# Performance work log

Hardware: AMD Instinct MI355X
Metric: run time of the kernel (lower is better)

The kernel has to match this reference:

```python
import jax, jax.numpy as jnp
import numpy as np

RADIUS = 0.1
NUM_POINT = 1024  # M centroids
SAMPLE_NUM = 32   # K neighbors per ball


def fps(xyz, m):
    """D-FPS farthest point sampling. xyz: (B,N,3) -> idx (B,m) int32."""
    B, N, _ = xyz.shape

    def step(carry, _):
        mind, far = carry  # mind (B,N), far (B,)
        centroid = jnp.take_along_axis(xyz, far[:, None, None], axis=1)  # (B,1,3)
        d = jnp.sum((xyz - centroid) ** 2, axis=-1)  # (B,N)
        mind = jnp.minimum(mind, d)
        nxt = jnp.argmax(mind, axis=1).astype(jnp.int32)
        return (mind, nxt), far

    init = (jnp.full((B, N), jnp.inf, xyz.dtype), jnp.zeros((B,), jnp.int32))
    _, idx = jax.lax.scan(step, init, None, length=m)
    return jnp.transpose(idx)  # (B,m)


def ball_query(new_xyz, xyz, radius, k):
    """First-k points within radius of each centroid, padded with first hit.
    new_xyz (B,M,3), xyz (B,N,3) -> (B,M,k) int32."""
    N = xyz.shape[1]
    d2 = jnp.sum((new_xyz[:, :, None, :] - xyz[:, None, :, :]) ** 2, axis=-1)  # (B,M,N)
    order = jnp.where(d2 < radius * radius, jnp.arange(N, dtype=jnp.int32)[None, None, :], N)
    neg, pos = jax.lax.top_k(-order, k)  # k smallest 'order' values -> first-k in-ball indices
    valid = (-neg) < N
    return jnp.where(valid, pos, pos[..., :1])


def setup_inputs() -> dict:
    key = jax.random.key(0)
    ks = jax.random.split(key, 12)
    B, N, C = 4, 16384, 64
    Cin = C + 3  # use_xyz=True
    points_xyz = jax.random.uniform(ks[0], (B, N, 3), dtype=jnp.float32)
    features = jax.random.normal(ks[1], (B, C, N), dtype=jnp.float32)
    s = lambda fan: 1.0 / np.sqrt(fan)
    inp = {
        "points_xyz": points_xyz,
        "features": features,
        "Wa": jax.random.normal(ks[2], (128, Cin), jnp.float32) * s(Cin),
        "ba": jnp.zeros((128,), jnp.float32),
        "Wb": jax.random.normal(ks[3], (128, 128), jnp.float32) * s(128),
        "bb": jnp.zeros((128,), jnp.float32),
        "Ws": jax.random.normal(ks[4], (128, Cin), jnp.float32) * s(Cin),
        "bs": jnp.zeros((128,), jnp.float32),
        "Wc": jax.random.normal(ks[5], (512, 128), jnp.float32) * s(128),
        "bc": jnp.zeros((512,), jnp.float32),
        "Wd": jax.random.normal(ks[6], (128, 512), jnp.float32) * s(512),
        "bd": jnp.zeros((128,), jnp.float32),
    }
    return inp


def _conv1x1(W, b, x):
    # pointwise conv over (B,C,M,K)
    return jnp.einsum('oc,bcmk->bomk', W, x) + b[None, :, None, None]


def reference(points_xyz, features, Wa, ba, Wb, bb, Ws, bs, Wc, bc, Wd, bd):
    idx = fps(points_xyz, NUM_POINT)  # (B,M)
    new_xyz = jnp.take_along_axis(points_xyz, idx[:, :, None], axis=1)  # (B,M,3)
    nidx = ball_query(new_xyz, points_xyz, RADIUS, SAMPLE_NUM)  # (B,M,K)
    # gather and relativize grouped xyz; gather grouped features
    grouped_xyz = jax.vmap(lambda p, i: p[i])(points_xyz, nidx) - new_xyz[:, :, None, :]  # (B,M,K,3)
    gfeat = jax.vmap(lambda f, i: f[:, i])(features, nidx)  # (B,C,M,K)
    g = jnp.concatenate([jnp.transpose(grouped_xyz, (0, 3, 1, 2)), gfeat], axis=1)  # (B,3+C,M,K)
    # mlp + shortcut residual + relu
    h = _conv1x1(Wb, bb, jax.nn.relu(_conv1x1(Wa, ba, g)))
    h = jax.nn.relu(h + _conv1x1(Ws, bs, g))
    # inverted mlp + identity residual + relu
    inv = _conv1x1(Wd, bd, jax.nn.relu(_conv1x1(Wc, bc, h)))
    out = jax.nn.relu(inv + h)
    pooled = jnp.max(out, axis=-1)  # max pool over K -> (B,128,M)
    return new_xyz, pooled, idx
```

## Files before the change

### kernel.cpp

```cpp
#include <hip/hip_runtime.h>

#define N_PTS   16384
#define M_CENT  1024
#define K_SMP   32
#define C_FEAT  64
#define NCELL   512

using bf16x8 = __attribute__((ext_vector_type(8))) short;
using s16x4  = __attribute__((ext_vector_type(4))) short;
using f32x4  = __attribute__((ext_vector_type(4))) float;

__device__ inline short f2bf(float f) {
    unsigned u = __float_as_uint(f);
    u += 0x7fffu + ((u >> 16) & 1u);
    return (short)(u >> 16);
}

#define DPP_SHR1 0x111
#define DPP_SHR2 0x112
#define DPP_SHR4 0x114
#define DPP_SHR8 0x118
#define DPP_BC15 0x142
#define DPP_BC31 0x143

template<int CTRL, int RM>
__device__ __forceinline__ float dppmax(float v) {
    int o = __builtin_amdgcn_update_dpp(__float_as_int(v), __float_as_int(v),
                                        CTRL, RM, 0xF, false);
    return fmaxf(v, __int_as_float(o));
}

__device__ __forceinline__ float wave64_fmax(float v) {
    v = dppmax<DPP_SHR1, 0xF>(v);
    v = dppmax<DPP_SHR2, 0xF>(v);
    v = dppmax<DPP_SHR4, 0xF>(v);
    v = dppmax<DPP_SHR8, 0xF>(v);
    v = dppmax<DPP_BC15, 0xA>(v);
    v = dppmax<DPP_BC31, 0xC>(v);
    return __int_as_float(__builtin_amdgcn_readlane(__float_as_int(v), 63));
}

__device__ __forceinline__ float row16_fmax(float v) {
    v = dppmax<DPP_SHR1, 0xF>(v);
    v = dppmax<DPP_SHR2, 0xF>(v);
    v = dppmax<DPP_SHR4, 0xF>(v);
    v = dppmax<DPP_SHR8, 0xF>(v);
    return __int_as_float(__builtin_amdgcn_readlane(__float_as_int(v), 15));
}

__device__ inline int hcell_of(float x, float y, float z) {
    int xi = (int)(x * 8.0f); xi = xi < 0 ? 0 : (xi > 7 ? 7 : xi);
    int yi = (int)(y * 8.0f); yi = yi < 0 ? 0 : (yi > 7 ? 7 : yi);
    int zi = (int)(z * 8.0f); zi = zi < 0 ? 0 : (zi > 7 ? 7 : zi);
    unsigned X[3] = {(unsigned)xi, (unsigned)yi, (unsigned)zi};
#pragma unroll
    for (unsigned Q = 4; Q > 1; Q >>= 1) {
        unsigned P = Q - 1;
#pragma unroll
        for (int i = 0; i < 3; ++i) {
            if (X[i] & Q) X[0] ^= P;
            else { unsigned t = (X[0] ^ X[i]) & P; X[0] ^= t; X[i] ^= t; }
        }
    }
    X[1] ^= X[0]; X[2] ^= X[1];
    unsigned t = 0;
#pragma unroll
    for (unsigned Q = 4; Q > 1; Q >>= 1)
        if (X[2] & Q) t ^= Q - 1;
    X[0] ^= t; X[1] ^= t; X[2] ^= t;
    int h = 0;
#pragma unroll
    for (int q = 2; q >= 0; --q)
        h = (h << 3) | (((X[0] >> q) & 1) << 2) | (((X[1] >> q) & 1) << 1) | ((X[2] >> q) & 1);
    return h;
}

__global__ __launch_bounds__(1024) void hist_kernel(
    const float* __restrict__ xyz, int* __restrict__ ghist)
{
    __shared__ int h[NCELL];
    const int b = blockIdx.x, tid = threadIdx.x;
    if (tid < NCELL) h[tid] = 0;
    __syncthreads();
    const float* P = xyz + (size_t)b * N_PTS * 3;
    for (int i = 0; i < 16; ++i) {
        const int p = tid + (i << 10);
        atomicAdd(&h[hcell_of(P[p*3], P[p*3+1], P[p*3+2])], 1);
    }
    __syncthreads();
    if (tid < NCELL) ghist[b * NCELL + tid] = h[tid];
}

__global__ __launch_bounds__(NCELL) void scan_kernel(
    const int* __restrict__ ghist, int* __restrict__ gbase)
{
    __shared__ int h[NCELL];
    const int b = blockIdx.x, t = threadIdx.x;
    h[t] = ghist[b * NCELL + t];
    __syncthreads();
    int s = 0;
    for (int i = 0; i < t; ++i) s += h[i];
    gbase[b * NCELL + t] = s;
}

__global__ __launch_bounds__(1024) void scatter_kernel(
    const float* __restrict__ xyz, int* __restrict__ gbase,
    float4* __restrict__ gsxyz)
{
    const int b = blockIdx.x, tid = threadIdx.x;
    const float* P = xyz + (size_t)b * N_PTS * 3;
    for (int i = 0; i < 16; ++i) {
        const int p = tid + (i << 10);
        float x = P[p*3], y = P[p*3+1], z = P[p*3+2];
        int c = hcell_of(x, y, z);
        int pos = atomicAdd(&gbase[b * NCELL + c], 1);
        gsxyz[(size_t)b * N_PTS + pos] = make_float4(x, y, z, __int_as_float(p));
    }
}

__global__ __launch_bounds__(1024) void fps_kernel(
    const float* __restrict__ xyz,
    const float4* __restrict__ gsxyz,
    float* __restrict__ newxyz_out,
    float* __restrict__ idxf_out)
{
#pragma clang fp contract(off)
    const int b = blockIdx.x, tid = threadIdx.x;
    const int wid = tid >> 6, lane = tid & 63;
    const float4* S = gsxyz + (size_t)b * N_PTS;

    __shared__ float2 xy[16 * 1024];
    __shared__ unsigned long long wkeys[2][16];
    __shared__ float4 wcoord[2][16];

    float z[16], mind[16];
    unsigned npk[8];
    float lox = 1e30f, hix = -1e30f, loy = 1e30f, hiy = -1e30f, loz = 1e30f, hiz = -1e30f;
#pragma unroll
    for (int i = 0; i < 16; ++i) {
        const float4 v = S[tid * 16 + i];
        xy[i * 1024 + tid] = make_float2(v.x, v.y);
        z[i] = v.z;
        mind[i] = __int_as_float(0x7f800000);
        const unsigned nr = 16383u - (unsigned)__float_as_int(v.w);
        if (i & 1) npk[i >> 1] |= nr << 16;
        else       npk[i >> 1]  = nr;
        lox = fminf(lox, v.x); hix = fmaxf(hix, v.x);
        loy = fminf(loy, v.y); hiy = fmaxf(hiy, v.y);
        loz = fminf(loz, v.z); hiz = fmaxf(hiz, v.z);
    }
    const unsigned pbx = (__float_as_uint(lox) >> 16) |
                         ((((__float_as_uint(hix) + 0xFFFFu) >> 16) << 16));
    const unsigned pby = (__float_as_uint(loy) >> 16) |
                         ((((__float_as_uint(hiy) + 0xFFFFu) >> 16) << 16));
    const unsigned pbz = (__float_as_uint(loz) >> 16) |
                         ((((__float_as_uint(hiz) + 0xFFFFu) >> 16) << 16));

    const float* P = xyz + (size_t)b * N_PTS * 3;
    float cx = P[0], cy = P[1], cz = P[2];
    if (tid == 0) {
        idxf_out[b * M_CENT] = 0.0f;
        newxyz_out[(b * M_CENT) * 3 + 0] = cx;
        newxyz_out[(b * M_CENT) * 3 + 1] = cy;
        newxyz_out[(b * M_CENT) * 3 + 2] = cz;
    }
    __syncthreads();

    float lmax = __int_as_float(0x7f800000);
    unsigned cwk_hi = 0u, cwk_lo = 0u;
    float cwx = 0.f, cwy = 0.f, cwz = 0.f;

    for (int j = 1; j < M_CENT; ++j) {
        const int par = j & 1;
        const float blox = __uint_as_float(pbx << 16);
        const float bhix = __uint_as_float(pbx & 0xFFFF0000u);
        const float bloy = __uint_as_float(pby << 16);
        const float bhiy = __uint_as_float(pby & 0xFFFF0000u);
        const float bloz = __uint_as_float(pbz << 16);
        const float bhiz = __uint_as_float(pbz & 0xFFFF0000u);
        float tx = fmaxf(fmaxf(blox - cx, cx - bhix), 0.0f);
        float ty = fmaxf(fmaxf(bloy - cy, cy - bhiy), 0.0f);
        float tz = fmaxf(fmaxf(bloz - cz, cz - bhiz), 0.0f);
        float lb = (tx * tx + ty * ty) + tz * tz;
        bool need = (lb * 0.999985f) < lmax;

        if (__any(need)) {
            float bv0 = -1.0f, bv1 = -1.0f;
#pragma unroll
            for (int i = 0; i < 16; i += 2) {
                const float2 p0 = xy[i * 1024 + tid];
                const float2 p1 = xy[(i + 1) * 1024 + tid];
                float dx0 = p0.x - cx, dy0 = p0.y - cy, dz0 = z[i] - cz;
                float dx1 = p1.x - cx, dy1 = p1.y - cy, dz1 = z[i + 1] - cz;
                float d0 = (dx0 * dx0 + dy0 * dy0) + dz0 * dz0;
                float d1 = (dx1 * dx1 + dy1 * dy1) + dz1 * dz1;
                float m0 = fminf(mind[i], d0);
                float m1 = fminf(mind[i + 1], d1);
                mind[i] = m0; mind[i + 1] = m1;
                bv0 = fmaxf(bv0, m0);
                bv1 = fmaxf(bv1, m1);
            }
            const float bv = fmaxf(bv0, bv1);
            lmax = bv;
            unsigned bk = 0u; float wz = 0.f;
#pragma unroll
            for (int i = 0; i < 16; ++i) {
                const unsigned nr = (i & 1) ? (npk[i >> 1] >> 16)
                                            : (npk[i >> 1] & 0xFFFFu);
                const unsigned nk = (nr << 4) | (unsigned)i;
                const bool c = (mind[i] == bv) && (nk >= bk);
                bk = c ? nk : bk;
                wz = c ? z[i] : wz;
            }
            const float wmax = wave64_fmax(bv);
            unsigned long long m = __ballot(bv == wmax);
            unsigned bestnk = 0u; int ol = 0;
            while (m) {
                const int l = (int)__ffsll(m) - 1;
                m &= m - 1;
                const unsigned nkl = (unsigned)__builtin_amdgcn_readlane((int)bk, l);
                if (nkl >= bestnk) { bestnk = nkl; ol = l; }
            }
            cwk_hi = __float_as_uint(wmax);
            cwk_lo = ((bestnk >> 4) << 8) | ((unsigned)wid << 4);
            const float2 pw = xy[(bestnk & 15u) * 1024 + (wid << 6) + ol];
            cwx = pw.x; cwy = pw.y;
            cwz = __int_as_float(__builtin_amdgcn_readlane(__float_as_int(wz), ol));
        }
        if (lane == 0) {
            wkeys[par][wid]  = ((unsigned long long)cwk_hi << 32) | cwk_lo;
            wcoord[par][wid] = make_float4(cwx, cwy, cwz, 0.f);
        }
        __syncthreads();

        const unsigned long long k = wkeys[par][lane & 15];
        const float vkey = __uint_as_float((unsigned)(k >> 32));
        const float vmax = row16_fmax(vkey);
        unsigned long long mm = __ballot(vkey == vmax) & 0xFFFFull;
        unsigned bestlo = 0u;
        while (mm) {
            const int l = (int)__ffsll(mm) - 1;
            mm &= mm - 1;
            const unsigned lo = (unsigned)__builtin_amdgcn_readlane((int)(unsigned)k, l);
            if (lo >= bestlo) bestlo = lo;
        }
        const int winw = (int)((bestlo >> 4) & 15u);
        const float4 wc = wcoord[par][winw];
        cx = wc.x; cy = wc.y; cz = wc.z;
        if (tid == 0) {
            const int orig = 16383 - (int)(bestlo >> 8);
            idxf_out[b * M_CENT + j] = (float)orig;
            newxyz_out[(b * M_CENT + j) * 3 + 0] = cx;
            newxyz_out[(b * M_CENT + j) * 3 + 1] = cy;
            newxyz_out[(b * M_CENT + j) * 3 + 2] = cz;
        }
    }
}

__global__ __launch_bounds__(256) void ball_kernel(
    const float* __restrict__ xyz,
    const float* __restrict__ newxyz,
    int* __restrict__ nidx)
{
#pragma clang fp contract(off)
    const float R2 = (float)(0.1 * 0.1);
    const int gw   = blockIdx.x * 4 + (threadIdx.x >> 6);
    const int lane = threadIdx.x & 63;
    const int b    = gw >> 10;
    const float* P = xyz + (size_t)b * N_PTS * 3;
    const float cx = newxyz[gw * 3 + 0];
    const float cy = newxyz[gw * 3 + 1];
    const float cz = newxyz[gw * 3 + 2];
    int* out = nidx + gw * K_SMP;

    int cnt = 0, first = -1;
    for (int base = 0; base < N_PTS; base += 64) {
        const int n = base + lane;
        float dx = P[n * 3 + 0] - cx;
        float dy = P[n * 3 + 1] - cy;
        float dz = P[n * 3 + 2] - cz;
        float xx = dx * dx, yy = dy * dy, zz = dz * dz;
        float d2 = (xx + yy) + zz;
        bool inb = d2 < R2;
        unsigned long long mask = __ballot(inb);
        if (mask) {
            if (first < 0) first = base + __ffsll(mask) - 1;
            int before = __popcll(mask & ((1ull << lane) - 1ull));
            int slot = cnt + before;
            if (inb && slot < K_SMP) out[slot] = n;
            cnt += __popcll(mask);
            if (cnt >= K_SMP) break;
        }
    }
    for (int s = cnt + lane; s < K_SMP; s += 64) out[s] = first;
}

__global__ void prep_w(const float* __restrict__ src, short* __restrict__ dst,
                       int OC, int IC, int ICP, int remap)
{
    int i = blockIdx.x * 256 + threadIdx.x;
    if (i >= OC * ICP) return;
    int oc = i / ICP, ic = i - oc * ICP;
    float v = 0.0f;
    if (remap) {
        if (ic < 64)      v = src[oc * IC + 3 + ic];
        else if (ic < 67) v = src[oc * IC + (ic - 64)];
    } else if (ic < IC)   v = src[oc * IC + ic];
    dst[i] = f2bf(v);
}

__global__ __launch_bounds__(256) void tfeat_kernel(
    const float* __restrict__ feat, float* __restrict__ featT)
{
    __shared__ float t[64][65];
    const int b = blockIdx.y;
    const int n0 = blockIdx.x * 64;
    for (int it = 0; it < 16; ++it) {
        int idx = it * 256 + threadIdx.x;
        int c = idx >> 6, n = idx & 63;
        t[c][n] = feat[((size_t)b * 64 + c) * N_PTS + n0 + n];
    }
    __syncthreads();
    for (int it = 0; it < 16; ++it) {
        int idx = it * 256 + threadIdx.x;
        int n = idx >> 6, c = idx & 63;
        featT[((size_t)b * N_PTS + n0 + n) * 64 + c] = t[c][n];
    }
}

__global__ __launch_bounds__(256, 2) void mlp_kernel(
    const float* __restrict__ xyz, const float* __restrict__ feat,
    const float* __restrict__ featT, int useT,
    const float* __restrict__ newxyz, const int* __restrict__ nidx,
    const short* __restrict__ WaB, const float* __restrict__ ba,
    const short* __restrict__ WbB, const float* __restrict__ bb,
    const short* __restrict__ WsB, const float* __restrict__ bs,
    const short* __restrict__ WcB, const float* __restrict__ bc,
    const short* __restrict__ WdB, const float* __restrict__ bd,
    float* __restrict__ pooled)
{
    __shared__ short Xt[64][104];
    __shared__ short Ht[64][136];
    __shared__ short Tt[64][136];

    const int tid = threadIdx.x;
    const int w = tid >> 6, l = tid & 63, l16 = l & 15, kg = l >> 4;
    const int cen0 = blockIdx.x * 2;
    const int b = cen0 >> 10;
    const int ocw = 32 * w;

    {
        const int col = tid >> 2, part = tid & 3;
        const int ci = cen0 + (col >> 5);
        const int nn = nidx[ci * K_SMP + (col & 31)];
        float v[16];
        if (useT) {
            const f32x4* src = (const f32x4*)(featT + ((size_t)b * N_PTS + nn) * 64 + part * 16);
            f32x4 f0 = src[0], f1 = src[1], f2 = src[2], f3 = src[3];
            v[0]=f0[0]; v[1]=f0[1]; v[2]=f0[2]; v[3]=f0[3];
            v[4]=f1[0]; v[5]=f1[1]; v[6]=f1[2]; v[7]=f1[3];
            v[8]=f2[0]; v[9]=f2[1]; v[10]=f2[2]; v[11]=f2[3];
            v[12]=f3[0]; v[13]=f3[1]; v[14]=f3[2]; v[15]=f3[3];
        } else {
            const float* F = feat + (size_t)b * C_FEAT * N_PTS + nn;
#pragma unroll
            for (int q = 0; q < 16; ++q) v[q] = F[(size_t)(part * 16 + q) * N_PTS];
        }
        bf16x8 h0, h1;
#pragma unroll
        for (int q = 0; q < 8; ++q) { h0[q] = f2bf(v[q]); h1[q] = f2bf(v[q + 8]); }
        *(bf16x8*)&Xt[col][part * 16]     = h0;
        *(bf16x8*)&Xt[col][part * 16 + 8] = h1;
        if (part == 0) {
            bf16x8 hx, zv;
#pragma unroll
            for (int q = 0; q < 8; ++q) { hx[q] = 0; zv[q] = 0; }
            hx[0] = f2bf(xyz[((size_t)b * N_PTS + nn) * 3 + 0] - newxyz[ci * 3 + 0]);
            hx[1] = f2bf(xyz[((size_t)b * N_PTS + nn) * 3 + 1] - newxyz[ci * 3 + 1]);
            hx[2] = f2bf(xyz[((size_t)b * N_PTS + nn) * 3 + 2] - newxyz[ci * 3 + 2]);
            *(bf16x8*)&Xt[col][64] = hx;
            *(bf16x8*)&Xt[col][72] = zv;
            *(bf16x8*)&Xt[col][80] = zv;
            *(bf16x8*)&Xt[col][88] = zv;
        }
    }
    __syncthreads();

    f32x4 accA[2][4], accS[2][4];
#pragma unroll
    for (int o = 0; o < 2; ++o)
#pragma unroll
        for (int ct = 0; ct < 4; ++ct) {
#pragma unroll
            for (int r = 0; r < 4; ++r) { accA[o][ct][r] = 0.f; accS[o][ct][r] = 0.f; }
        }
#pragma unroll
    for (int k = 0; k < 3; ++k) {
        bf16x8 xb[4];
#pragma unroll
        for (int ct = 0; ct < 4; ++ct)
            xb[ct] = *(const bf16x8*)&Xt[ct * 16 + l16][k * 32 + kg * 8];
#pragma unroll
        for (int o = 0; o < 2; ++o) {
            const int row = ocw + o * 16 + l16;
            bf16x8 wa  = *(const bf16x8*)(WaB + row * 96 + k * 32 + kg * 8);
            bf16x8 wsv = *(const bf16x8*)(WsB + row * 96 + k * 32 + kg * 8);
#pragma unroll
            for (int ct = 0; ct < 4; ++ct) {
                accA[o][ct] = __builtin_amdgcn_mfma_f32_16x16x32_bf16(wa,  xb[ct], accA[o][ct], 0, 0, 0);
                accS[o][ct] = __builtin_amdgcn_mfma_f32_16x16x32_bf16(wsv, xb[ct], accS[o][ct], 0, 0, 0);
            }
        }
    }
#pragma unroll
    for (int o = 0; o < 2; ++o) {
        const f32x4 bav = *(const f32x4*)(ba + ocw + o * 16 + kg * 4);
#pragma unroll
        for (int ct = 0; ct < 4; ++ct) {
            s16x4 hv;
#pragma unroll
            for (int r = 0; r < 4; ++r) hv[r] = f2bf(fmaxf(accA[o][ct][r] + bav[r], 0.f));
            *(s16x4*)&Ht[ct * 16 + l16][ocw + o * 16 + kg * 4] = hv;
        }
    }
    __syncthreads();

    f32x4 accB[2][4];
#pragma unroll
    for (int o = 0; o < 2; ++o)
#pragma unroll
        for (int ct = 0; ct < 4; ++ct) {
#pragma unroll
            for (int r = 0; r < 4; ++r) accB[o][ct][r] = 0.f;
        }
#pragma unroll
    for (int k = 0; k < 4; ++k) {
        bf16x8 xb[4];
#pragma unroll
        for (int ct = 0; ct < 4; ++ct)
            xb[ct] = *(const bf16x8*)&Ht[ct * 16 + l16][k * 32 + kg * 8];
#pragma unroll
        for (int o = 0; o < 2; ++o) {
            const int row = ocw + o * 16 + l16;
            bf16x8 wbv = *(const bf16x8*)(WbB + row * 128 + k * 32 + kg * 8);
#pragma unroll
            for (int ct = 0; ct < 4; ++ct)
                accB[o][ct] = __builtin_amdgcn_mfma_f32_16x16x32_bf16(wbv, xb[ct], accB[o][ct], 0, 0, 0);
        }
    }
    f32x4 hreg[2][4];
#pragma unroll
    for (int o = 0; o < 2; ++o) {
        const f32x4 bbv = *(const f32x4*)(bb + ocw + o * 16 + kg * 4);
        const f32x4 bsv = *(const f32x4*)(bs + ocw + o * 16 + kg * 4);
#pragma unroll
        for (int ct = 0; ct < 4; ++ct) {
#pragma unroll
            for (int r = 0; r < 4; ++r)
                hreg[o][ct][r] = fmaxf((accB[o][ct][r] + bbv[r]) + (accS[o][ct][r] + bsv[r]), 0.f);
        }
    }
    __syncthreads();
#pragma unroll
    for (int o = 0; o < 2; ++o)
#pragma unroll
        for (int ct = 0; ct < 4; ++ct) {
            s16x4 hv;
#pragma unroll
            for (int r = 0; r < 4; ++r) hv[r] = f2bf(hreg[o][ct][r]);
            *(s16x4*)&Ht[ct * 16 + l16][ocw + o * 16 + kg * 4] = hv;
        }
    __syncthreads();

    f32x4 accD[2][4];
#pragma unroll
    for (int o = 0; o < 2; ++o)
#pragma unroll
        for (int ct = 0; ct < 4; ++ct) {
#pragma unroll
            for (int r = 0; r < 4; ++r) accD[o][ct][r] = 0.f;
        }
    for (int cc = 0; cc < 4; ++cc) {
        f32x4 accC[2][4];
#pragma unroll
        for (int o = 0; o < 2; ++o)
#pragma unroll
            for (int ct = 0; ct < 4; ++ct) {
#pragma unroll
                for (int r = 0; r < 4; ++r) accC[o][ct][r] = 0.f;
            }
#pragma unroll
        for (int k = 0; k < 4; ++k) {
            bf16x8 xb[4];
#pragma unroll
            for (int ct = 0; ct < 4; ++ct)
                xb[ct] = *(const bf16x8*)&Ht[ct * 16 + l16][k * 32 + kg * 8];
#pragma unroll
            for (int o = 0; o < 2; ++o) {
                const int row = cc * 128 + ocw + o * 16 + l16;
                bf16x8 wcv = *(const bf16x8*)(WcB + row * 128 + k * 32 + kg * 8);
#pragma unroll
                for (int ct = 0; ct < 4; ++ct)
                    accC[o][ct] = __builtin_amdgcn_mfma_f32_16x16x32_bf16(wcv, xb[ct], accC[o][ct], 0, 0, 0);
            }
        }
        __syncthreads();
#pragma unroll
        for (int o = 0; o < 2; ++o) {
            const f32x4 bcv = *(const f32x4*)(bc + cc * 128 + ocw + o * 16 + kg * 4);
#pragma unroll
            for (int ct = 0; ct < 4; ++ct) {
                s16x4 tv;
#pragma unroll
                for (int r = 0; r < 4; ++r) tv[r] = f2bf(fmaxf(accC[o][ct][r] + bcv[r], 0.f));
                *(s16x4*)&Tt[ct * 16 + l16][ocw + o * 16 + kg * 4] = tv;
            }
        }
        __syncthreads();
#pragma unroll
        for (int k = 0; k < 4; ++k) {
            bf16x8 tb[4];
#pragma unroll
            for (int ct = 0; ct < 4; ++ct)
                tb[ct] = *(const bf16x8*)&Tt[ct * 16 + l16][k * 32 + kg * 8];
#pragma unroll
            for (int o = 0; o < 2; ++o) {
                const int row = ocw + o * 16 + l16;
                bf16x8 wdv = *(const bf16x8*)(WdB + row * 512 + cc * 128 + k * 32 + kg * 8);
#pragma unroll
                for (int ct = 0; ct < 4; ++ct)
                    accD[o][ct] = __builtin_amdgcn_mfma_f32_16x16x32_bf16(wdv, tb[ct], accD[o][ct], 0, 0, 0);
            }
        }
    }

    const int m0 = cen0 & 1023;
#pragma unroll
    for (int o = 0; o < 2; ++o) {
        const f32x4 bdv = *(const f32x4*)(bd + ocw + o * 16 + kg * 4);
#pragma unroll
        for (int r = 0; r < 4; ++r) {
            float a0 = fmaxf((accD[o][0][r] + bdv[r]) + hreg[o][0][r], 0.f);
            float a1 = fmaxf((accD[o][1][r] + bdv[r]) + hreg[o][1][r], 0.f);
            float a2 = fmaxf((accD[o][2][r] + bdv[r]) + hreg[o][2][r], 0.f);
            float a3 = fmaxf((accD[o][3][r] + bdv[r]) + hreg[o][3][r], 0.f);
            float u0 = fmaxf(a0, a1), u1 = fmaxf(a2, a3);
#pragma unroll
            for (int off = 1; off < 16; off <<= 1) {
                u0 = fmaxf(u0, __shfl_xor(u0, off));
                u1 = fmaxf(u1, __shfl_xor(u1, off));
            }
            if (l16 == 0) {
                const int oc = ocw + o * 16 + kg * 4 + r;
                pooled[((size_t)b * 128 + oc) * 1024 + m0]     = u0;
                pooled[((size_t)b * 128 + oc) * 1024 + m0 + 1] = u1;
            }
        }
    }
}

extern "C" void kernel_launch(void* const* d_in, const int* in_sizes, int n_in,
                              void* d_out, int out_size, void* d_ws, size_t ws_size,
                              hipStream_t stream)
{
    const float* xyz  = (const float*)d_in[0];
    const float* feat = (const float*)d_in[1];
    const float* Wa = (const float*)d_in[2];   const float* ba = (const float*)d_in[3];
    const float* Wb = (const float*)d_in[4];   const float* bb = (const float*)d_in[5];
    const float* Ws = (const float*)d_in[6];   const float* bs = (const float*)d_in[7];
    const float* Wc = (const float*)d_in[8];   const float* bc = (const float*)d_in[9];
    const float* Wd = (const float*)d_in[10];  const float* bd = (const float*)d_in[11];

    float* out    = (float*)d_out;
    float* newxyz = out;
    float* pooled = out + 4 * 1024 * 3;
    float* idxf   = pooled + 4 * 128 * 1024;

    char* ws = (char*)d_ws;
    float4* gsxyz = (float4*)ws;
    int*    nidx  = (int*)ws;
    short* WaB = (short*)(ws + (1 << 20));
    short* WsB = WaB + 128 * 96;
    short* WbB = WsB + 128 * 96;
    short* WcB = WbB + 128 * 128;
    short* WdB = WcB + 512 * 128;
    int*   ghist = (int*)(WdB + 128 * 512);
    int*   gbase = ghist + 4 * NCELL;
    float* featT = (float*)(ws + (2 << 20));

    const size_t need = (size_t)(2 << 20) + (size_t)4 * N_PTS * 64 * 4;
    const int useT = (ws_size >= need) ? 1 : 0;

    prep_w<<<(128 *  96 + 255) / 256, 256, 0, stream>>>(Wa, WaB, 128,  67,  96, 1);
    prep_w<<<(128 *  96 + 255) / 256, 256, 0, stream>>>(Ws, WsB, 128,  67,  96, 1);
    prep_w<<<(128 * 128 + 255) / 256, 256, 0, stream>>>(Wb, WbB, 128, 128, 128, 0);
    prep_w<<<(512 * 128 + 255) / 256, 256, 0, stream>>>(Wc, WcB, 512, 128, 128, 0);
    prep_w<<<(128 * 512 + 255) / 256, 256, 0, stream>>>(Wd, WdB, 128, 512, 512, 0);
    if (useT) tfeat_kernel<<<dim3(N_PTS / 64, 4), 256, 0, stream>>>(feat, featT);

    hist_kernel   <<<4, 1024,  0, stream>>>(xyz, ghist);
    scan_kernel   <<<4, NCELL, 0, stream>>>(ghist, gbase);
    scatter_kernel<<<4, 1024,  0, stream>>>(xyz, gbase, gsxyz);

    fps_kernel<<<4, 1024, 0, stream>>>(xyz, gsxyz, newxyz, idxf);
    ball_kernel<<<1024, 256, 0, stream>>>(xyz, newxyz, nidx);
    mlp_kernel<<<2048, 256, 0, stream>>>(xyz, feat, featT, useT, newxyz, nidx,
                                         WaB, ba, WbB, bb, WsB, bs,
                                         WcB, bc, WdB, bd, pooled);
}
```

Baseline: 1.473 ms.

## Split FPS argmax into value reduction then winner-only index resolution

```diff
diff --git a/kernel.cpp b/kernel.cpp
--- a/kernel.cpp
+++ b/kernel.cpp
@@ -130,8 +130,9 @@
     const float4* S = gsxyz + (size_t)b * N_PTS;
 
     __shared__ float2 xy[16 * 1024];
-    __shared__ unsigned long long wkeys[2][16];
-    __shared__ float4 wcoord[2][16];
+    __shared__ float wval[16];
+    __shared__ unsigned wkey2[16];
+    __shared__ float4 wcoord[16];
 
     float z[16], mind[16];
     unsigned npk[8];
@@ -149,12 +150,6 @@
         loy = fminf(loy, v.y); hiy = fmaxf(hiy, v.y);
         loz = fminf(loz, v.z); hiz = fmaxf(hiz, v.z);
     }
-    const unsigned pbx = (__float_as_uint(lox) >> 16) |
-                         ((((__float_as_uint(hix) + 0xFFFFu) >> 16) << 16));
-    const unsigned pby = (__float_as_uint(loy) >> 16) |
-                         ((((__float_as_uint(hiy) + 0xFFFFu) >> 16) << 16));
-    const unsigned pbz = (__float_as_uint(loz) >> 16) |
-                         ((((__float_as_uint(hiz) + 0xFFFFu) >> 16) << 16));
 
     const float* P = xyz + (size_t)b * N_PTS * 3;
     float cx = P[0], cy = P[1], cz = P[2];
@@ -167,24 +162,15 @@
     __syncthreads();
 
     float lmax = __int_as_float(0x7f800000);
-    unsigned cwk_hi = 0u, cwk_lo = 0u;
-    float cwx = 0.f, cwy = 0.f, cwz = 0.f;
+    float wmax = __int_as_float(0x7f800000);
 
     for (int j = 1; j < M_CENT; ++j) {
-        const int par = j & 1;
-        const float blox = __uint_as_float(pbx << 16);
-        const float bhix = __uint_as_float(pbx & 0xFFFF0000u);
-        const float bloy = __uint_as_float(pby << 16);
-        const float bhiy = __uint_as_float(pby & 0xFFFF0000u);
-        const float bloz = __uint_as_float(pbz << 16);
-        const float bhiz = __uint_as_float(pbz & 0xFFFF0000u);
-        float tx = fmaxf(fmaxf(blox - cx, cx - bhix), 0.0f);
-        float ty = fmaxf(fmaxf(bloy - cy, cy - bhiy), 0.0f);
-        float tz = fmaxf(fmaxf(bloz - cz, cz - bhiz), 0.0f);
+        float tx = fmaxf(fmaxf(lox - cx, cx - hix), 0.0f);
+        float ty = fmaxf(fmaxf(loy - cy, cy - hiy), 0.0f);
+        float tz = fmaxf(fmaxf(loz - cz, cz - hiz), 0.0f);
         float lb = (tx * tx + ty * ty) + tz * tz;
-        bool need = (lb * 0.999985f) < lmax;
-
-        if (__any(need)) {
+
+        if (__any((lb * 0.999985f) < lmax)) {
             float bv0 = -1.0f, bv1 = -1.0f;
 #pragma unroll
             for (int i = 0; i < 16; i += 2) {
@@ -200,56 +186,63 @@
                 bv0 = fmaxf(bv0, m0);
                 bv1 = fmaxf(bv1, m1);
             }
-            const float bv = fmaxf(bv0, bv1);
-            lmax = bv;
+            lmax = fmaxf(bv0, bv1);
+            wmax = wave64_fmax(lmax);
+        }
+        if (lane == 0) wval[wid] = wmax;
+        __syncthreads();
+
+        const float vkey = wval[lane & 15];
+        const float gmax = row16_fmax(vkey);
+        const unsigned long long tm = __ballot(vkey == gmax) & 0xFFFFull;
+
+        if ((tm >> wid) & 1ull) {
             unsigned bk = 0u; float wz = 0.f;
 #pragma unroll
             for (int i = 0; i < 16; ++i) {
                 const unsigned nr = (i & 1) ? (npk[i >> 1] >> 16)
                                             : (npk[i >> 1] & 0xFFFFu);
-                const unsigned nk = (nr << 4) | (unsigned)i;
-                const bool c = (mind[i] == bv) && (nk >= bk);
+                const unsigned nk = ((nr << 4) | (unsigned)i) + 1u;
+                const bool c = (mind[i] == gmax) && (nk >= bk);
                 bk = c ? nk : bk;
                 wz = c ? z[i] : wz;
             }
-            const float wmax = wave64_fmax(bv);
-            unsigned long long m = __ballot(bv == wmax);
+            unsigned long long lm = __ballot(bk != 0u);
             unsigned bestnk = 0u; int ol = 0;
-            while (m) {
-                const int l = (int)__ffsll(m) - 1;
-                m &= m - 1;
+            while (lm) {
+                const int l = (int)__ffsll(lm) - 1;
+                lm &= lm - 1;
                 const unsigned nkl = (unsigned)__builtin_amdgcn_readlane((int)bk, l);
                 if (nkl >= bestnk) { bestnk = nkl; ol = l; }
             }
-            cwk_hi = __float_as_uint(wmax);
-            cwk_lo = ((bestnk >> 4) << 8) | ((unsigned)wid << 4);
-            const float2 pw = xy[(bestnk & 15u) * 1024 + (wid << 6) + ol];
-            cwx = pw.x; cwy = pw.y;
-            cwz = __int_as_float(__builtin_amdgcn_readlane(__float_as_int(wz), ol));
-        }
-        if (lane == 0) {
-            wkeys[par][wid]  = ((unsigned long long)cwk_hi << 32) | cwk_lo;
-            wcoord[par][wid] = make_float4(cwx, cwy, cwz, 0.f);
+            const unsigned dec   = bestnk - 1u;
+            const unsigned bi    = dec & 15u;
+            const unsigned norig = dec >> 4;
+            const float2 pw = xy[bi * 1024 + (wid << 6) + ol];
+            const float wzr = __int_as_float(
+                __builtin_amdgcn_readlane(__float_as_int(wz), ol));
+            if (lane == 0) {
+                wkey2[wid]  = norig + 1u;
+                wcoord[wid] = make_float4(pw.x, pw.y, wzr,
+                                          (float)(16383 - (int)norig));
+            }
         }
         __syncthreads();
 
-        const unsigned long long k = wkeys[par][lane & 15];
-        const float vkey = __uint_as_float((unsigned)(k >> 32));
-        const float vmax = row16_fmax(vkey);
-        unsigned long long mm = __ballot(vkey == vmax) & 0xFFFFull;
-        unsigned bestlo = 0u;
-        while (mm) {
-            const int l = (int)__ffsll(mm) - 1;
-            mm &= mm - 1;
-            const unsigned lo = (unsigned)__builtin_amdgcn_readlane((int)(unsigned)k, l);
-            if (lo >= bestlo) bestlo = lo;
-        }
-        const int winw = (int)((bestlo >> 4) & 15u);
-        const float4 wc = wcoord[par][winw];
+        int winw;
+        if (__popcll(tm) == 1) {
+            winw = (int)__ffsll(tm) - 1;
+        } else {
+            const int sl = lane & 15;
+            const float fk = ((tm >> sl) & 1ull) ? (float)wkey2[sl] : 0.0f;
+            const float fm = row16_fmax(fk);
+            unsigned long long mm = __ballot(fk == fm) & 0xFFFFull;
+            winw = (int)__ffsll(mm) - 1;
+        }
+        const float4 wc = wcoord[winw];
         cx = wc.x; cy = wc.y; cz = wc.z;
         if (tid == 0) {
-            const int orig = 16383 - (int)(bestlo >> 8);
-            idxf_out[b * M_CENT + j] = (float)orig;
+            idxf_out[b * M_CENT + j] = wc.w;
             newxyz_out[(b * M_CENT + j) * 3 + 0] = cx;
             newxyz_out[(b * M_CENT + j) * 3 + 1] = cy;
             newxyz_out[(b * M_CENT + j) * 3 + 2] = cz;
```

After: 1.541 ms. +4.6%, slower.
